# Performance work log

Hardware: AMD Instinct MI355X
Metric: run time of the kernel (lower is better)

Reference implementation:

```python
import jax, jax.numpy as jnp
import numpy as np

N_HEADS = 32
N_KV_HEADS = 8
HEAD_DIM = 128
DIM = 4096
ROPE_THETA = 500000.0
BSZ, SEQLEN = 4, 1024


def _rope(t, cos, sin):
    # t: [B,S,H,hd]; cos/sin: [S,hd//2]
    te = t[..., 0::2]
    to = t[..., 1::2]
    c = cos[None, :, None, :]
    s = sin[None, :, None, :]
    out = jnp.stack([te * c - to * s, te * s + to * c], axis=-1)
    return out.reshape(t.shape)


def setup_inputs() -> dict:
    key = jax.random.key(0)
    ks = jax.random.split(key, 8)
    scale = 1.0 / np.sqrt(DIM)
    x = jax.random.normal(ks[0], (BSZ, SEQLEN, DIM), dtype=jnp.float32)
    wq = jax.random.normal(ks[1], (DIM, N_HEADS * HEAD_DIM), dtype=jnp.float32) * scale
    wk = jax.random.normal(ks[2], (DIM, N_KV_HEADS * HEAD_DIM), dtype=jnp.float32) * scale
    wv = jax.random.normal(ks[3], (DIM, N_KV_HEADS * HEAD_DIM), dtype=jnp.float32) * scale
    wo = jax.random.normal(ks[4], (N_HEADS * HEAD_DIM, DIM), dtype=jnp.float32) * scale
    # rotary tables: freqs_cis[s, j] = exp(i * s * theta^(-2j/hd))
    inv_freq = 1.0 / (ROPE_THETA ** (np.arange(0, HEAD_DIM, 2, dtype=np.float32) / HEAD_DIM))
    ang = np.outer(np.arange(SEQLEN, dtype=np.float32), inv_freq)
    freqs_cos = jnp.asarray(np.cos(ang), dtype=jnp.float32)
    freqs_sin = jnp.asarray(np.sin(ang), dtype=jnp.float32)
    # additive causal mask: 0 on/below diag, -inf above
    causal_mask = jnp.triu(jnp.full((SEQLEN, SEQLEN), -jnp.inf, dtype=jnp.float32), k=1)
    return {"x": x, "wq": wq, "wk": wk, "wv": wv, "wo": wo,
            "freqs_cos": freqs_cos, "freqs_sin": freqs_sin,
            "causal_mask": causal_mask, "fixed_point_iter": 0, "start_pos": 0}


def reference(x, wq, wk, wv, wo, freqs_cos, freqs_sin, causal_mask, fixed_point_iter, start_pos):
    B, S, _ = x.shape
    n_rep = N_HEADS // N_KV_HEADS
    xq = (x @ wq).reshape(B, S, N_HEADS, HEAD_DIM)
    xk = (x @ wk).reshape(B, S, N_KV_HEADS, HEAD_DIM)
    xv = (x @ wv).reshape(B, S, N_KV_HEADS, HEAD_DIM)
    xq = _rope(xq, freqs_cos, freqs_sin)
    xk = _rope(xk, freqs_cos, freqs_sin)
    # start_pos == 0 prefill: cache slice [:start_pos+S] equals freshly written xk/xv
    keys = jnp.repeat(xk, n_rep, axis=2)    # [B,S,H,hd]
    values = jnp.repeat(xv, n_rep, axis=2)
    scores = jnp.einsum('bqhd,bkhd->bhqk', xq, keys) / np.sqrt(HEAD_DIM)
    scores = scores + causal_mask  # broadcast [S,S]
    probs = jax.nn.softmax(scores.astype(jnp.float32), axis=-1).astype(xq.dtype)
    out = jnp.einsum('bhqk,bkhd->bqhd', probs, values)
    out = out.reshape(B, S, N_HEADS * HEAD_DIM)
    return out @ wo
```

## Files before the change

kernel.cpp:

```cpp
#include <hip/hip_runtime.h>

#define BSZ_  4
#define SEQ_  1024
#define NH_   32
#define NKVH_ 8
#define HD_   128
#define DIM_  4096
#define NTOK_ (BSZ_ * SEQ_)
#define QKVW_ 6144

typedef float  floatx4  __attribute__((ext_vector_type(4)));
typedef float  floatx16 __attribute__((ext_vector_type(16)));
typedef __bf16 bf16x8   __attribute__((ext_vector_type(8)));
typedef unsigned short ushortx8 __attribute__((ext_vector_type(8)));

__device__ __forceinline__ float fast_exp2(float x) {
  return __builtin_amdgcn_exp2f(x);
}

__device__ __forceinline__ unsigned short f2bf_bits(float f) {
  unsigned int u = __float_as_uint(f);
  u += 0x7FFFu + ((u >> 16) & 1u);
  return (unsigned short)(u >> 16);
}
__device__ __forceinline__ unsigned int pack_bf2_rne(float lo, float hi_) {
  return (unsigned int)f2bf_bits(lo) | ((unsigned int)f2bf_bits(hi_) << 16);
}
__device__ __forceinline__ unsigned int pack_bf2_trunc(float lo, float hi_) {
  return __builtin_amdgcn_perm(__float_as_uint(hi_), __float_as_uint(lo), 0x07060302u);
}

__device__ __forceinline__ void gld16(const void* g, void* l) {
  __builtin_amdgcn_global_load_lds(
      (const __attribute__((address_space(1))) void*)g,
      (__attribute__((address_space(3))) void*)l, 16, 0, 0);
}

__global__ __launch_bounds__(256)
void xconv(const float* __restrict__ X, unsigned short* __restrict__ XB)
{
  size_t i = ((size_t)blockIdx.x * 256 + threadIdx.x) * 4;
  float4 v = *(const float4*)&X[i];
  ushort4 o;
  o.x = f2bf_bits(v.x); o.y = f2bf_bits(v.y);
  o.z = f2bf_bits(v.z); o.w = f2bf_bits(v.w);
  *(ushort4*)&XB[i] = o;
}

__global__ __launch_bounds__(256)
void wtrans(const float* __restrict__ W, unsigned short* __restrict__ WT,
            int K, int N)
{
  __shared__ unsigned short T[32][36];
  const int k0 = blockIdx.y * 32, n0 = blockIdx.x * 32;
  const int t = threadIdx.x;
  {
    int kr = t >> 3, nc = (t & 7) * 4;
    float4 v = *(const float4*)&W[(size_t)(k0 + kr) * N + n0 + nc];
    T[kr][nc + 0] = f2bf_bits(v.x);
    T[kr][nc + 1] = f2bf_bits(v.y);
    T[kr][nc + 2] = f2bf_bits(v.z);
    T[kr][nc + 3] = f2bf_bits(v.w);
  }
  __syncthreads();
  {
    int nr = t >> 3, kc = (t & 7) * 4;
    ushort4 o;
    o.x = T[kc + 0][nr]; o.y = T[kc + 1][nr];
    o.z = T[kc + 2][nr]; o.w = T[kc + 3][nr];
    *(ushort4*)&WT[(size_t)(n0 + nr) * K + k0 + kc] = o;
  }
}

__global__ __launch_bounds__(256)
void vtrans2(const unsigned short* __restrict__ qkv, unsigned short* __restrict__ VT)
{
  __shared__ unsigned short T[32][36];
  const int bh = blockIdx.z;
  const int s0 = blockIdx.x * 32, d0 = blockIdx.y * 32;
  const int b = bh >> 3, kvh = bh & 7;
  const int t = threadIdx.x;
  {
    int sr = t >> 3, dc = (t & 7) * 4;
    ushort4 v = *(const ushort4*)&qkv[(size_t)(b * SEQ_ + s0 + sr) * QKVW_ + 5120 + kvh * HD_ + d0 + dc];
    T[sr][dc + 0] = v.x; T[sr][dc + 1] = v.y;
    T[sr][dc + 2] = v.z; T[sr][dc + 3] = v.w;
  }
  __syncthreads();
  {
    int dr = t >> 3, sc = (t & 7) * 4;
    ushort4 o;
    o.x = T[sc + 0][dr]; o.y = T[sc + 1][dr];
    o.z = T[sc + 2][dr]; o.w = T[sc + 3][dr];
    *(ushort4*)&VT[((size_t)bh * HD_ + d0 + dr) * SEQ_ + s0 + sc] = o;
  }
}

__global__ __launch_bounds__(256)
void rope2(unsigned int* __restrict__ t, const float* __restrict__ cosf,
           const float* __restrict__ sinf, int shift, int stride_u32, int base_u32)
{
  int idx = blockIdx.x * 256 + threadIdx.x;
  int tok = idx >> shift;
  int rem = idx & ((1 << shift) - 1);
  int d2  = idx & 63;
  int pos = tok & (SEQ_ - 1);
  unsigned int* p = &t[(size_t)tok * stride_u32 + base_u32 + rem];
  unsigned int pv = *p;
  float xe = __uint_as_float(pv << 16);
  float xo = __uint_as_float(pv & 0xFFFF0000u);
  float cv = cosf[pos * 64 + d2];
  float sv = sinf[pos * 64 + d2];
  float oe = xe * cv - xo * sv;
  float oo = xe * sv + xo * cv;
  *p = pack_bf2_rne(oe, oo);
}

template<bool OUT_BF16>
__global__ __launch_bounds__(1024, 4)
void gemm_w16(const unsigned short* __restrict__ A,
              const unsigned short* __restrict__ B,
              void* __restrict__ Cout, int M, int N, int K)
{
  __shared__ __align__(16) unsigned short As[4][256][32];
  __shared__ __align__(16) unsigned short Bs[4][256][32];

  const int tid  = threadIdx.x;
  const int w    = tid >> 6;
  const int lane = tid & 63;
  const int l16  = lane & 15;
  const int quad = lane >> 4;
  const int wr   = w >> 2;
  const int wc   = w & 3;

  int wg = blockIdx.x;
  const int q8 = gridDim.x >> 3;
  wg = (wg & 7) * q8 + (wg >> 3);
  const int nbx = N >> 8;
  const int bm = (wg / nbx) * 256;
  const int bn = (wg % nbx) * 256;

  const int srow = tid >> 2;
  const int scs  = (tid & 3) ^ ((srow >> 1) & 3);
  const unsigned short* Ag = &A[(size_t)(bm + srow) * K + scs * 8];
  const unsigned short* Bg = &B[(size_t)(bn + srow) * K + scs * 8];
  char* AsW = (char*)&As[0][0][0] + w * 1024;
  char* BsW = (char*)&Bs[0][0][0] + w * 1024;

  const int ntiles = K >> 5;

  auto stage = [&](int kt, int buf) {
    size_t ko = (size_t)kt << 5;
    gld16(Ag + ko, AsW + buf * 16384);
    gld16(Bg + ko, BsW + buf * 16384);
  };

  floatx4 acc[4][4];
#pragma unroll
  for (int i = 0; i < 4; i++)
#pragma unroll
    for (int j = 0; j < 4; j++) acc[i][j] = (floatx4){0.f, 0.f, 0.f, 0.f};

  const int cfr = quad ^ ((l16 >> 1) & 3);
  const unsigned short* ArF = &As[0][wr * 64][cfr * 8];
  const unsigned short* BrF = &Bs[0][wc * 64][cfr * 8];

  stage(0, 0); stage(1, 1); stage(2, 2);
  asm volatile("s_waitcnt vmcnt(4)" ::: "memory");
  __builtin_amdgcn_s_barrier();

#pragma unroll 1
  for (int t = 0; t < ntiles; t++) {
    const int buf = t & 3;

    bf16x8 af[4], bfr[4];
    {
      const unsigned short* Ab = ArF + (size_t)buf * (256 * 32) + l16 * 32;
      const unsigned short* Bb = BrF + (size_t)buf * (256 * 32) + l16 * 32;
#pragma unroll
      for (int i = 0; i < 4; i++) af[i]  = *(const bf16x8*)&Ab[i * (16 * 32)];
#pragma unroll
      for (int j = 0; j < 4; j++) bfr[j] = *(const bf16x8*)&Bb[j * (16 * 32)];
    }

    {
      int pk = (t + 3 < ntiles) ? t + 3 : 0;
      stage(pk, (t + 3) & 3);
    }

    __builtin_amdgcn_s_setprio(1);
#pragma unroll
    for (int i = 0; i < 4; i++)
#pragma unroll
      for (int j = 0; j < 4; j++)
        acc[i][j] = __builtin_amdgcn_mfma_f32_16x16x32_bf16(af[i], bfr[j], acc[i][j], 0, 0, 0);
    __builtin_amdgcn_s_setprio(0);

    asm volatile("s_waitcnt vmcnt(4)" ::: "memory");
    __builtin_amdgcn_s_barrier();
  }

  asm volatile("s_waitcnt vmcnt(0)" ::: "memory");

#pragma unroll
  for (int i = 0; i < 4; i++)
#pragma unroll
    for (int j = 0; j < 4; j++)
#pragma unroll
      for (int r = 0; r < 4; r++) {
        size_t row = bm + wr * 64 + i * 16 + quad * 4 + r;
        size_t col = bn + wc * 64 + j * 16 + l16;
        if (OUT_BF16)
          ((unsigned short*)Cout)[row * N + col] = f2bf_bits(acc[i][j][r]);
        else
          ((float*)Cout)[row * N + col] = acc[i][j][r];
      }
}

__global__ __launch_bounds__(256, 2)
void flash_attn2(const unsigned short* __restrict__ qkv,
                 const unsigned short* __restrict__ vt,
                 unsigned short* __restrict__ o)
{
  __shared__ __align__(16) unsigned short S_[4][8192];
  unsigned short* Ks = &S_[0][0];
  unsigned short* Vs = &S_[1][0];

  const int bid = blockIdx.x;
  const int grp = bid >> 7;
  const int idx = bid & 127;
  const int qt = (grp == 0) ? 3 : (grp == 1) ? 2 : (grp == 2) ? 0 : 1;
  const int h = idx & 31, b = idx >> 5;

  const int kvh = h >> 2;
  const int tid = threadIdx.x, w = tid >> 6, lane = tid & 63;
  const int l31 = lane & 31, hi = lane >> 5;
  const int qb = qt * 256, qw = qb + w * 64;
  unsigned short* Ps = &S_[2][0] + w * 4096;

  const float CEXP = (float)(0.08838834764831845 * 1.4426950408889634);

  bf16x8 qf[2][8];
#pragma unroll
  for (int t2 = 0; t2 < 2; t2++) {
    const unsigned short* qrow =
        &qkv[(size_t)(b * SEQ_ + qw + t2 * 32 + l31) * QKVW_ + h * HD_ + hi * 8];
#pragma unroll
    for (int s = 0; s < 8; s++)
      qf[t2][s] = *(const bf16x8*)&qrow[s * 16];
  }

  floatx16 oa[2][4];
#pragma unroll
  for (int t2 = 0; t2 < 2; t2++)
#pragma unroll
    for (int dt = 0; dt < 4; dt++)
#pragma unroll
      for (int r = 0; r < 16; r++) oa[t2][dt][r] = 0.f;

  float ms[2] = {-3.0e38f, -3.0e38f};
  float ls[2] = {0.f, 0.f};

  const int nk = qb + 256;
  const int qmaxw = qw + 63;

  ushortx8 kreg[4], vreg[4];
  const size_t kg0 = (size_t)(b * SEQ_) * QKVW_ + 4096 + kvh * HD_;
  const size_t vg0 = ((size_t)(b * NKVH_ + kvh) * HD_) * SEQ_;
  const int krow = tid >> 4, kc = tid & 15;
  const int vrow = tid >> 3, vc = tid & 7;

  auto issue_loads = [&](int kb) {
    const size_t gb = kg0 + (size_t)kb * QKVW_;
#pragma unroll
    for (int it = 0; it < 4; it++)
      kreg[it] = *(const ushortx8*)&qkv[gb + (size_t)(it * 16 + krow) * QKVW_ + kc * 8];
    const size_t vb = vg0 + kb;
#pragma unroll
    for (int it = 0; it < 4; it++)
      vreg[it] = *(const ushortx8*)&vt[vb + (size_t)(it * 32 + vrow) * SEQ_ + vc * 8];
  };
  auto write_lds = [&]() {
#pragma unroll
    for (int it = 0; it < 4; it++) {
      int key = it * 16 + krow;
      *(ushortx8*)&Ks[key * 128 + ((kc ^ (key & 15)) * 8)] = kreg[it];
    }
#pragma unroll
    for (int it = 0; it < 4; it++) {
      int d = it * 32 + vrow;
      *(ushortx8*)&Vs[d * 64 + ((vc ^ (d & 7)) * 8)] = vreg[it];
    }
  };

  issue_loads(0);

  for (int kb_ = 0; kb_ < nk; kb_ += 64) {
    __syncthreads();
    write_lds();
    if (kb_ + 64 < nk) issue_loads(kb_ + 64);
    asm volatile("s_waitcnt lgkmcnt(0)" ::: "memory");
    __builtin_amdgcn_s_barrier();

    if (kb_ <= qmaxw) {
      const bool needmask = (kb_ + 63 > qw);

#pragma unroll
      for (int t2 = 0; t2 < 2; t2++) {
        floatx16 sc[2];
#pragma unroll
        for (int r = 0; r < 16; r++) { sc[0][r] = 0.f; sc[1][r] = 0.f; }
        __builtin_amdgcn_s_setprio(1);
#pragma unroll
        for (int s = 0; s < 8; s++) {
          int c = 2 * s + hi;
          bf16x8 k0 = *(const bf16x8*)&Ks[l31 * 128 + ((c ^ (l31 & 15)) * 8)];
          bf16x8 k1 = *(const bf16x8*)&Ks[(32 + l31) * 128 + ((c ^ ((32 + l31) & 15)) * 8)];
          sc[0] = __builtin_amdgcn_mfma_f32_32x32x16_bf16(k0, qf[t2][s], sc[0], 0, 0, 0);
          sc[1] = __builtin_amdgcn_mfma_f32_32x32x16_bf16(k1, qf[t2][s], sc[1], 0, 0, 0);
        }
        __builtin_amdgcn_s_setprio(0);

        if (needmask) {
          const int q = qw + t2 * 32 + l31;
#pragma unroll
          for (int k2 = 0; k2 < 2; k2++)
#pragma unroll
            for (int r = 0; r < 16; r++) {
              int key = kb_ + k2 * 32 + (r & 3) + 8 * (r >> 2) + 4 * hi;
              if (key > q) sc[k2][r] = -3.0e38f;
            }
        }

        float mx0 = sc[0][0], mx1 = sc[0][1];
#pragma unroll
        for (int r = 2; r < 16; r += 2) { mx0 = fmaxf(mx0, sc[0][r]); mx1 = fmaxf(mx1, sc[0][r + 1]); }
#pragma unroll
        for (int r = 0; r < 16; r += 2) { mx0 = fmaxf(mx0, sc[1][r]); mx1 = fmaxf(mx1, sc[1][r + 1]); }
        float mx = fmaxf(mx0, mx1);
        mx = fmaxf(mx, __shfl_xor(mx, 32));
        float mxs = mx * CEXP;

        float mn, alpha;
        if (__all(mxs - ms[t2] <= 8.0f)) {
          mn = ms[t2]; alpha = 1.0f;
        } else {
          mn = fmaxf(ms[t2], mxs);
          alpha = fast_exp2(ms[t2] - mn);
          ms[t2] = mn;
        }

        float rs0 = 0.f, rs1 = 0.f;
        const int qloc = t2 * 32 + l31;
#pragma unroll
        for (int k2 = 0; k2 < 2; k2++) {
          unsigned int pk[8];
#pragma unroll
          for (int r = 0; r < 16; r += 2) {
            float p0 = fast_exp2(__builtin_fmaf(sc[k2][r],     CEXP, -mn));
            float p1 = fast_exp2(__builtin_fmaf(sc[k2][r + 1], CEXP, -mn));
            rs0 += p0; rs1 += p1;
            pk[r >> 1] = pack_bf2_trunc(p0, p1);
          }
#pragma unroll
          for (int rq = 0; rq < 4; rq++) {
            int keyoff = k2 * 32 + 8 * rq + 4 * hi;
            int c = keyoff >> 3;
            uint2 val = {pk[rq * 2], pk[rq * 2 + 1]};
            *(uint2*)&Ps[qloc * 64 + ((c ^ (qloc & 7)) * 8) + (keyoff & 7)] = val;
          }
        }
        float rs = rs0 + rs1;
        rs += __shfl_xor(rs, 32);
        ls[t2] = ls[t2] * alpha + rs;

        if (__any(alpha != 1.0f)) {
#pragma unroll
          for (int dt = 0; dt < 4; dt++)
#pragma unroll
            for (int r = 0; r < 16; r++) oa[t2][dt][r] *= alpha;
        }
      }

      __builtin_amdgcn_s_setprio(1);
#pragma unroll
      for (int ks = 0; ks < 4; ks++) {
        int c = 2 * ks + hi;
        bf16x8 pf0, pf1;
        {
          int q0l = l31;
          int q1l = 32 + l31;
          pf0 = *(const bf16x8*)&Ps[q0l * 64 + ((c ^ (q0l & 7)) * 8)];
          pf1 = *(const bf16x8*)&Ps[q1l * 64 + ((c ^ (q1l & 7)) * 8)];
        }
#pragma unroll
        for (int dt = 0; dt < 4; dt++) {
          int d = dt * 32 + l31;
          bf16x8 vf = *(const bf16x8*)&Vs[d * 64 + ((c ^ (d & 7)) * 8)];
          oa[0][dt] = __builtin_amdgcn_mfma_f32_32x32x16_bf16(vf, pf0, oa[0][dt], 0, 0, 0);
          oa[1][dt] = __builtin_amdgcn_mfma_f32_32x32x16_bf16(vf, pf1, oa[1][dt], 0, 0, 0);
        }
      }
      __builtin_amdgcn_s_setprio(0);
    }
  }

  __syncthreads();
  unsigned short* patch = &S_[w][0];
  float inv[2] = {1.0f / ls[0], 1.0f / ls[1]};
#pragma unroll
  for (int t2 = 0; t2 < 2; t2++) {
    const int qloc = t2 * 32 + l31;
#pragma unroll
    for (int dt = 0; dt < 4; dt++)
#pragma unroll
      for (int rq = 0; rq < 4; rq++) {
        float a0 = oa[t2][dt][rq * 4 + 0] * inv[t2];
        float a1 = oa[t2][dt][rq * 4 + 1] * inv[t2];
        float a2 = oa[t2][dt][rq * 4 + 2] * inv[t2];
        float a3 = oa[t2][dt][rq * 4 + 3] * inv[t2];
        int doff = dt * 32 + 8 * rq + 4 * hi;
        int c = doff >> 3;
        uint2 val = {pack_bf2_rne(a0, a1), pack_bf2_rne(a2, a3)};
        *(uint2*)&patch[qloc * 128 + ((c ^ (qloc & 7)) * 8) + (doff & 7)] = val;
      }
  }
#pragma unroll
  for (int it = 0; it < 16; it++) {
    int idx2 = it * 64 + lane;
    int row = idx2 >> 4, c = idx2 & 15;
    int cc = (c & 7) ^ (row & 7);
    int cs = (c & 8) | cc;
    ushortx8 vv = *(const ushortx8*)&patch[row * 128 + cs * 8];
    *(ushortx8*)&o[(size_t)(b * SEQ_ + qb + w * 64 + row) * 4096 + h * HD_ + c * 8] = vv;
  }
}

extern "C" void kernel_launch(void* const* d_in, const int* in_sizes, int n_in,
                              void* d_out, int out_size, void* d_ws, size_t ws_size,
                              hipStream_t stream)
{
  const float* x  = (const float*)d_in[0];
  const float* wq = (const float*)d_in[1];
  const float* wk = (const float*)d_in[2];
  const float* wv = (const float*)d_in[3];
  const float* wo = (const float*)d_in[4];
  const float* fc = (const float*)d_in[5];
  const float* fs = (const float*)d_in[6];
  float* out = (float*)d_out;

  unsigned short* xb    = (unsigned short*)d_ws;
  unsigned short* wqkvT = xb    + (size_t)NTOK_ * DIM_;
  unsigned short* qkvb  = wqkvT + (size_t)QKVW_ * DIM_;
  unsigned short* vtb   = qkvb  + (size_t)NTOK_ * QKVW_;
  unsigned short* ab    = xb;
  unsigned short* woT   = wqkvT;

  dim3 blk(256);

  xconv<<<(NTOK_ * DIM_ / 4) / 256, blk, 0, stream>>>(x, xb);
  wtrans<<<dim3(DIM_ / 32, DIM_ / 32), blk, 0, stream>>>(wq, wqkvT, DIM_, DIM_);
  wtrans<<<dim3((NKVH_ * HD_) / 32, DIM_ / 32), blk, 0, stream>>>(wk, wqkvT + (size_t)4096 * DIM_, DIM_, NKVH_ * HD_);
  wtrans<<<dim3((NKVH_ * HD_) / 32, DIM_ / 32), blk, 0, stream>>>(wv, wqkvT + (size_t)5120 * DIM_, DIM_, NKVH_ * HD_);

  gemm_w16<true><<<dim3((QKVW_ / 256) * (NTOK_ / 256)), dim3(1024), 0, stream>>>(
      xb, wqkvT, qkvb, NTOK_, QKVW_, DIM_);

  wtrans<<<dim3(DIM_ / 32, DIM_ / 32), blk, 0, stream>>>(wo, woT, DIM_, DIM_);

  rope2<<<(NTOK_ * 2048) / 256, blk, 0, stream>>>((unsigned int*)qkvb, fc, fs, 11, 3072, 0);
  rope2<<<(NTOK_ * 512) / 256, blk, 0, stream>>>((unsigned int*)qkvb, fc, fs, 9, 3072, 2048);

  vtrans2<<<dim3(SEQ_ / 32, HD_ / 32, BSZ_ * NKVH_), blk, 0, stream>>>(qkvb, vtb);

  flash_attn2<<<dim3((SEQ_ / 256) * NH_ * BSZ_), blk, 0, stream>>>(qkvb, vtb, ab);

  gemm_w16<false><<<dim3((DIM_ / 256) * (NTOK_ / 256)), dim3(1024), 0, stream>>>(
      ab, woT, out, NTOK_, DIM_, DIM_);
}
```

Baseline: 703.6 us.

## Switch GEMM to BK=64 tiles with double buffering and 8-way XOR swizzle

Replaces the 4-stage BK=32 pipeline in the bf16 GEMM with a 2-stage BK=64 pipeline. Each tile now takes two 16-byte async loads per operand and runs two MFMA rounds per barrier, so barriers and loop overhead per unit of K are halved. The LDS swizzle moves to an 8-chunk XOR pattern to suit the wider rows. The trade-off is a shallower prefetch (one tile ahead instead of three) and a full vmcnt(0) wait each iteration, which may expose more memory latency.

```diff
diff --git a/kernel.cpp b/kernel.cpp
--- a/kernel.cpp
+++ b/kernel.cpp
@@ -118,12 +118,12 @@
 
 template<bool OUT_BF16>
 __global__ __launch_bounds__(1024, 4)
-void gemm_w16(const unsigned short* __restrict__ A,
-              const unsigned short* __restrict__ B,
-              void* __restrict__ Cout, int M, int N, int K)
-{
-  __shared__ __align__(16) unsigned short As[4][256][32];
-  __shared__ __align__(16) unsigned short Bs[4][256][32];
+void gemm_bk64(const unsigned short* __restrict__ A,
+               const unsigned short* __restrict__ B,
+               void* __restrict__ Cout, int M, int N, int K)
+{
+  __shared__ __align__(16) unsigned short As[2][256][64];
+  __shared__ __align__(16) unsigned short Bs[2][256][64];
 
   const int tid  = threadIdx.x;
   const int w    = tid >> 6;
@@ -140,19 +140,22 @@
   const int bm = (wg / nbx) * 256;
   const int bn = (wg % nbx) * 256;
 
-  const int srow = tid >> 2;
-  const int scs  = (tid & 3) ^ ((srow >> 1) & 3);
-  const unsigned short* Ag = &A[(size_t)(bm + srow) * K + scs * 8];
-  const unsigned short* Bg = &B[(size_t)(bn + srow) * K + scs * 8];
+  const int srow = tid >> 3;
+  const int sc8  = (tid & 7) ^ (srow & 7);
+  const unsigned short* Ag = &A[(size_t)(bm + srow) * K + sc8 * 8];
+  const unsigned short* Bg = &B[(size_t)(bn + srow) * K + sc8 * 8];
+  const size_t rhalf = (size_t)128 * K;
   char* AsW = (char*)&As[0][0][0] + w * 1024;
   char* BsW = (char*)&Bs[0][0][0] + w * 1024;
 
-  const int ntiles = K >> 5;
+  const int ntiles = K >> 6;
 
   auto stage = [&](int kt, int buf) {
-    size_t ko = (size_t)kt << 5;
-    gld16(Ag + ko, AsW + buf * 16384);
-    gld16(Bg + ko, BsW + buf * 16384);
+    size_t ko = (size_t)kt << 6;
+    gld16(Ag + ko,         AsW + buf * 32768);
+    gld16(Ag + ko + rhalf, AsW + buf * 32768 + 16384);
+    gld16(Bg + ko,         BsW + buf * 32768);
+    gld16(Bg + ko + rhalf, BsW + buf * 32768 + 16384);
   };
 
   floatx4 acc[4][4];
@@ -161,33 +164,30 @@
 #pragma unroll
     for (int j = 0; j < 4; j++) acc[i][j] = (floatx4){0.f, 0.f, 0.f, 0.f};
 
-  const int cfr = quad ^ ((l16 >> 1) & 3);
-  const unsigned short* ArF = &As[0][wr * 64][cfr * 8];
-  const unsigned short* BrF = &Bs[0][wc * 64][cfr * 8];
-
-  stage(0, 0); stage(1, 1); stage(2, 2);
-  asm volatile("s_waitcnt vmcnt(4)" ::: "memory");
+  const int cf0 = (quad)     ^ (l16 & 7);
+  const int cf1 = (4 + quad) ^ (l16 & 7);
+
+  stage(0, 0);
+  asm volatile("s_waitcnt vmcnt(0)" ::: "memory");
   __builtin_amdgcn_s_barrier();
 
 #pragma unroll 1
   for (int t = 0; t < ntiles; t++) {
-    const int buf = t & 3;
+    const int buf = t & 1;
+
+    {
+      int pk = (t + 1 < ntiles) ? t + 1 : 0;
+      stage(pk, (t + 1) & 1);
+    }
+
+    const unsigned short* Ab = &As[buf][wr * 64 + l16][0];
+    const unsigned short* Bb = &Bs[buf][wc * 64 + l16][0];
 
     bf16x8 af[4], bfr[4];
-    {
-      const unsigned short* Ab = ArF + (size_t)buf * (256 * 32) + l16 * 32;
-      const unsigned short* Bb = BrF + (size_t)buf * (256 * 32) + l16 * 32;
-#pragma unroll
-      for (int i = 0; i < 4; i++) af[i]  = *(const bf16x8*)&Ab[i * (16 * 32)];
-#pragma unroll
-      for (int j = 0; j < 4; j++) bfr[j] = *(const bf16x8*)&Bb[j * (16 * 32)];
-    }
-
-    {
-      int pk = (t + 3 < ntiles) ? t + 3 : 0;
-      stage(pk, (t + 3) & 3);
-    }
-
+#pragma unroll
+    for (int i = 0; i < 4; i++) af[i]  = *(const bf16x8*)&Ab[i * (16 * 64) + cf0 * 8];
+#pragma unroll
+    for (int j = 0; j < 4; j++) bfr[j] = *(const bf16x8*)&Bb[j * (16 * 64) + cf0 * 8];
     __builtin_amdgcn_s_setprio(1);
 #pragma unroll
     for (int i = 0; i < 4; i++)
@@ -196,11 +196,21 @@
         acc[i][j] = __builtin_amdgcn_mfma_f32_16x16x32_bf16(af[i], bfr[j], acc[i][j], 0, 0, 0);
     __builtin_amdgcn_s_setprio(0);
 
-    asm volatile("s_waitcnt vmcnt(4)" ::: "memory");
+#pragma unroll
+    for (int i = 0; i < 4; i++) af[i]  = *(const bf16x8*)&Ab[i * (16 * 64) + cf1 * 8];
+#pragma unroll
+    for (int j = 0; j < 4; j++) bfr[j] = *(const bf16x8*)&Bb[j * (16 * 64) + cf1 * 8];
+    __builtin_amdgcn_s_setprio(1);
+#pragma unroll
+    for (int i = 0; i < 4; i++)
+#pragma unroll
+      for (int j = 0; j < 4; j++)
+        acc[i][j] = __builtin_amdgcn_mfma_f32_16x16x32_bf16(af[i], bfr[j], acc[i][j], 0, 0, 0);
+    __builtin_amdgcn_s_setprio(0);
+
+    asm volatile("s_waitcnt vmcnt(0)" ::: "memory");
     __builtin_amdgcn_s_barrier();
   }
-
-  asm volatile("s_waitcnt vmcnt(0)" ::: "memory");
 
 #pragma unroll
   for (int i = 0; i < 4; i++)
@@ -463,7 +473,7 @@
   wtrans<<<dim3((NKVH_ * HD_) / 32, DIM_ / 32), blk, 0, stream>>>(wk, wqkvT + (size_t)4096 * DIM_, DIM_, NKVH_ * HD_);
   wtrans<<<dim3((NKVH_ * HD_) / 32, DIM_ / 32), blk, 0, stream>>>(wv, wqkvT + (size_t)5120 * DIM_, DIM_, NKVH_ * HD_);
 
-  gemm_w16<true><<<dim3((QKVW_ / 256) * (NTOK_ / 256)), dim3(1024), 0, stream>>>(
+  gemm_bk64<true><<<dim3((QKVW_ / 256) * (NTOK_ / 256)), dim3(1024), 0, stream>>>(
       xb, wqkvT, qkvb, NTOK_, QKVW_, DIM_);
 
   wtrans<<<dim3(DIM_ / 32, DIM_ / 32), blk, 0, stream>>>(wo, woT, DIM_, DIM_);
@@ -475,6 +485,6 @@
 
   flash_attn2<<<dim3((SEQ_ / 256) * NH_ * BSZ_), blk, 0, stream>>>(qkvb, vtb, ab);
 
-  gemm_w16<false><<<dim3((DIM_ / 256) * (NTOK_ / 256)), dim3(1024), 0, stream>>>(
+  gemm_bk64<false><<<dim3((DIM_ / 256) * (NTOK_ / 256)), dim3(1024), 0, stream>>>(
       ab, woT, out, NTOK_, DIM_, DIM_);
 }
```

Result: slower. 719.4 us (+2.3%).
